# Performance work log

Measured on AMD Instinct MI355X. Metric: run time of the kernel, lower is better.

## Reference

```python
import jax, jax.numpy as jnp
import numpy as np
from jax import lax

SPAN = 11
K = 2 * SPAN + 1          # 23 -> 529 offsets
SIG_RGB = 0.1
SIG_XY = 6.0
LAM = 0.15
B, C, H, W = 2, 3, 160, 160


def _patches(x):
    """x: (N, C, H, W) -> (N, C, K, K, H, W), zero-padded.
    patch[di, dj] at pixel (i, j) equals x[i + di - SPAN, j + dj - SPAN],
    matching the torch module's shifted-slice double loop (dx = di - SPAN)."""
    n, c, h, w = x.shape
    xp = jnp.pad(x, ((0, 0), (0, 0), (SPAN, SPAN), (SPAN, SPAN)))

    def get(off):
        di = off // K
        dj = off % K
        return lax.dynamic_slice(xp, (0, 0, di, dj), (n, c, h, w))

    p = jax.vmap(get)(jnp.arange(K * K))              # (K*K, N, C, H, W)
    return p.reshape(K, K, n, c, h, w).transpose(2, 3, 0, 1, 4, 5)


def setup_inputs() -> dict:
    key = jax.random.key(0)
    k1, k2, k3, k4, k5 = jax.random.split(key, 5)
    logit = jax.random.normal(k1, (B, C, H, W), jnp.float32)
    target = jax.random.randint(k2, (B, H, W), 0, C)
    # small-magnitude image so exp(-0.5*(x - patch/0.1)^2) does not fully underflow
    image = jax.random.uniform(k3, (B, 3, H, W), jnp.float32) * 0.1
    source_map = (jax.random.uniform(k4, (B, 1, H, W)) > 0.5).astype(jnp.float32)
    destination_map = (jax.random.uniform(k5, (B, H, W)) > 0.5).astype(jnp.float32)
    return dict(logit=logit, target=target, image=image,
                source_map=source_map, destination_map=destination_map)


def _gcrf(image, y_hat, source_map, m_dst):
    b, c, h, w = y_hat.shape
    img_p = _patches(image)                                  # (B,3,K,K,H,W)
    valid = _patches(jnp.ones((1, 1, h, w), image.dtype))[0, 0]  # (K,K,H,W) in-bounds mask
    # NOTE: faithful to source bug: only the shifted feature is divided by sigma
    drgb = image[:, :, None, None] - img_p / SIG_RGB
    k_rgb = jnp.exp(-0.5 * jnp.sum(drgb * drgb, axis=1))     # (B,K,K,H,W)
    ii, jj = jnp.meshgrid(jnp.arange(h, dtype=image.dtype),
                          jnp.arange(w, dtype=image.dtype), indexing='ij')
    idx = jnp.stack([ii, jj])[None]                          # (1,2,H,W)
    idx_p = _patches(idx)[0]                                 # (2,K,K,H,W)
    dxy = idx[0][:, None, None] - idx_p / SIG_XY
    k_xy = jnp.exp(-0.5 * jnp.sum(dxy * dxy, axis=0))        # (K,K,H,W)
    kmat = (k_rgb + k_xy[None]) * valid[None]                # out-of-bounds offsets stay 0
    m_src = _patches(source_map)[:, 0]                       # (B,K,K,H,W)
    Kg = kmat * m_src * m_dst[:, None, None]                 # gated kernel
    U = _patches(y_hat)                                      # (B,C,K,K,H,W)
    Egy = jnp.einsum('bcijhw,bijhw->bchw', U, Kg)            # sum over window
    temp = jnp.einsum('bchw,bdhw->bcd', Egy, y_hat)          # (B,C,C)
    Moff = 1.0 - jnp.eye(c, dtype=y_hat.dtype)               # off-diagonal compatibility
    return jnp.sum(Moff * temp) / (b * h * w)


def reference(logit, target, image, source_map, destination_map):
    y_hat = jax.nn.softmax(logit, axis=1)
    m_dst = 1.0 - destination_map
    L_gcrf = _gcrf(image, y_hat, source_map, m_dst)
    logp = jax.nn.log_softmax(logit, axis=1)
    L_ce = -jnp.take_along_axis(logp, target[:, None], axis=1)[:, 0]  # (B,H,W)
    L_ce = jnp.mean(L_ce * destination_map)
    return L_ce + LAM * L_gcrf
```

## Files before the change

kernel.cpp:

```cpp
#include <hip/hip_runtime.h>

#define Bn 2
#define Cn 3
#define Hn 160
#define Wn 160
#define SPANc 11
#define Kc 23
#define HWn (Hn * Wn)
#define PW 182
#define PP (PW * PW)
#define LAMc 0.15f
#define INVN (1.0f / (float)(Bn * HWn))
#define TJ 32
#define Gc 4
#define TI 32
#define NROW (TI + Kc - 1)
#define NREC (NROW * TJ)
#define CEXP (-0.72134752f)
#define CX   (14.42695041f)
#define CA   (0.72134752f)
#define NPREP ((Bn * PP + 255) / 256)

__device__ __forceinline__ float wave_reduce64(float v) {
#pragma unroll
    for (int off = 32; off > 0; off >>= 1) v += __shfl_down(v, off, 64);
    return v;
}

__device__ __forceinline__ unsigned int bf16pk(float a, float b) {
    unsigned int ua = __float_as_uint(a), ub = __float_as_uint(b);
    ua += 0x7fffu + ((ua >> 16) & 1u);
    ub += 0x7fffu + ((ub >> 16) & 1u);
    return (ua & 0xffff0000u) | (ub >> 16);
}

__global__ __launch_bounds__(256) void prep_kernel(
    const float* __restrict__ logit, const int* __restrict__ target,
    const float* __restrict__ image, const float* __restrict__ srcmap,
    const float* __restrict__ dstmap, uint4* __restrict__ gU4,
    float4* __restrict__ cvec, float* __restrict__ pc, float* __restrict__ out)
{
    int idx = blockIdx.x * 256 + threadIdx.x;
    float ce = 0.0f;
    if (idx < Bn * PP) {
        int b   = idx / PP;
        int rem = idx - b * PP;
        int ip  = rem / PW;
        int jp  = rem - ip * PW;
        int i = ip - SPANc, j = jp - SPANc;
        if ((unsigned)i < (unsigned)Hn && (unsigned)j < (unsigned)Wn) {
            int r = i * Wn + j;
            int p = b * HWn + r;
            const float* lg = logit + (size_t)b * Cn * HWn + r;
            float l0 = lg[0], l1 = lg[HWn], l2 = lg[2 * HWn];
            float m = fmaxf(l0, fmaxf(l1, l2));
            float e0 = __expf(l0 - m), e1 = __expf(l1 - m), e2 = __expf(l2 - m);
            float s = e0 + e1 + e2;
            float inv = 1.0f / s;
            float y0 = e0 * inv, y1 = e1 * inv, y2 = e2 * inv;
            float lse = m + __logf(s);

            const float* im = image + (size_t)b * 3 * HWn + r;
            float p0 = im[0], p1 = im[HWn], p2 = im[2 * HWn];
            float sv = srcmap[p];
            float dv = dstmap[p];

            float B = (p0 * p0 + p1 * p1 + p2 * p2) * (100.0f * CA);
            gU4[idx] = make_uint4(bf16pk(p0, p1), bf16pk(p2, -B),
                                  bf16pk(sv * y0, sv * y1), bf16pk(sv * y2, 0.0f));

            float md = LAMc * (1.0f - dv) * INVN;
            cvec[p] = make_float4(md * (1.0f - y0), md * (1.0f - y1),
                                  md * (1.0f - y2), 0.0f);

            int t = target[p];
            float lt = (t == 0) ? l0 : ((t == 1) ? l1 : l2);
            ce = (lse - lt) * dv * INVN;
        } else {
            gU4[idx] = make_uint4(0u, 0u, 0u, 0u);
        }
    }
    if (idx == 0) out[0] = 0.0f;

    float v = wave_reduce64(ce);
    __shared__ float wsum[4];
    int tid = threadIdx.x;
    if ((tid & 63) == 0) wsum[tid >> 6] = v;
    __syncthreads();
    if (tid == 0) pc[blockIdx.x] = wsum[0] + wsum[1] + wsum[2] + wsum[3];
}

template<bool XY>
__device__ __forceinline__ void tap(float p0, float p1, float p2, float mB,
                                    float q0, float q1, float q2,
                                    float c0s, float c1s, float c2s, float mA,
                                    bool xy_on, float dy2, float dxv,
                                    float& e0, float& e1, float& e2)
{
    float e = fmaf(c0s, p0, fmaf(c1s, p1, fmaf(c2s, p2, mB)));
    float k = exp2f(e + mA);
    if constexpr (XY) {
        if (xy_on) k += exp2f(fmaf(dxv, dxv, dy2) * CEXP);
    }
    e0 = fmaf(k, q0, e0);
    e1 = fmaf(k, q1, e1);
    e2 = fmaf(k, q2, e2);
}

template<bool XY>
__device__ __forceinline__ void window_loop(
    const uint4* sU4, int lbase,
    const float* c0s, const float* c1s, const float* c2s, const float* mA,
    bool xy_on, float dy2, float fi0, float eg[Gc][3])
{
#pragma unroll
    for (int r = 0; r < 3; ++r) {
        uint4 ru = sU4[lbase + r * TJ];
        float p0 = __uint_as_float(ru.x & 0xffff0000u);
        float p1 = __uint_as_float(ru.x << 16);
        float p2 = __uint_as_float(ru.y & 0xffff0000u);
        float mB = __uint_as_float(ru.y << 16);
        float q0 = __uint_as_float(ru.z & 0xffff0000u);
        float q1 = __uint_as_float(ru.z << 16);
        float q2 = __uint_as_float(ru.w & 0xffff0000u);
        float dxb = XY ? (fi0 - (fi0 + (float)(r - SPANc)) * (1.0f / 6.0f)) : 0.0f;
#pragma unroll
        for (int c = 0; c < 3; ++c) {
            if (c > r) continue;
            tap<XY>(p0, p1, p2, mB, q0, q1, q2, c0s[c], c1s[c], c2s[c], mA[c],
                    xy_on, dy2, dxb + (float)c, eg[c][0], eg[c][1], eg[c][2]);
        }
    }
#pragma unroll 2
    for (int r = 3; r <= 22; ++r) {
        uint4 ru = sU4[lbase + r * TJ];
        float p0 = __uint_as_float(ru.x & 0xffff0000u);
        float p1 = __uint_as_float(ru.x << 16);
        float p2 = __uint_as_float(ru.y & 0xffff0000u);
        float mB = __uint_as_float(ru.y << 16);
        float q0 = __uint_as_float(ru.z & 0xffff0000u);
        float q1 = __uint_as_float(ru.z << 16);
        float q2 = __uint_as_float(ru.w & 0xffff0000u);
        float dxb = XY ? (fi0 - (fi0 + (float)(r - SPANc)) * (1.0f / 6.0f)) : 0.0f;
#pragma unroll
        for (int c = 0; c < Gc; ++c) {
            tap<XY>(p0, p1, p2, mB, q0, q1, q2, c0s[c], c1s[c], c2s[c], mA[c],
                    xy_on, dy2, dxb + (float)c, eg[c][0], eg[c][1], eg[c][2]);
        }
    }
#pragma unroll
    for (int r = 23; r <= 25; ++r) {
        uint4 ru = sU4[lbase + r * TJ];
        float p0 = __uint_as_float(ru.x & 0xffff0000u);
        float p1 = __uint_as_float(ru.x << 16);
        float p2 = __uint_as_float(ru.y & 0xffff0000u);
        float mB = __uint_as_float(ru.y << 16);
        float q0 = __uint_as_float(ru.z & 0xffff0000u);
        float q1 = __uint_as_float(ru.z << 16);
        float q2 = __uint_as_float(ru.w & 0xffff0000u);
        float dxb = XY ? (fi0 - (fi0 + (float)(r - SPANc)) * (1.0f / 6.0f)) : 0.0f;
#pragma unroll
        for (int c = 1; c < Gc; ++c) {
            if (c < r - 22) continue;
            tap<XY>(p0, p1, p2, mB, q0, q1, q2, c0s[c], c1s[c], c2s[c], mA[c],
                    xy_on, dy2, dxb + (float)c, eg[c][0], eg[c][1], eg[c][2]);
        }
    }
}

__global__ __launch_bounds__(256, 4) void gcrf_kernel(
    const uint4* __restrict__ gU4, const float4* __restrict__ cvec,
    const float* __restrict__ pc, float* __restrict__ out)
{
    __shared__ uint4 sU4[NREC];

    int tx = threadIdx.x;
    int ty = threadIdx.y;
    int tid = ty * TJ + tx;
    int jx = blockIdx.x;
    int j  = jx * TJ + tx;
    int by = blockIdx.y;
    int b  = by / 5;
    int it = by - b * 5;
    int i0g = it * TI + ty * Gc;
    int dj = blockIdx.z;

    size_t g0 = (size_t)b * PP + (size_t)(it * TI) * PW + (jx * TJ + dj);
    for (int n = tid; n < NREC; n += 256) {
        int rr = n >> 5, cc = n & 31;
        sU4[n] = gU4[g0 + (size_t)rr * PW + cc];
    }
    __syncthreads();

    int lbase = ty * Gc * TJ + tx;
    float c0s[Gc], c1s[Gc], c2s[Gc], mA[Gc];
#pragma unroll
    for (int c = 0; c < Gc; ++c) {
        uint4 cu = sU4[lbase + (c + SPANc) * TJ];
        float cc0 = __uint_as_float(cu.x & 0xffff0000u);
        float cc1 = __uint_as_float(cu.x << 16);
        float cc2 = __uint_as_float(cu.y & 0xffff0000u);
        c0s[c] = cc0 * CX; c1s[c] = cc1 * CX; c2s[c] = cc2 * CX;
        mA[c] = -CA * fmaf(cc0, cc0, fmaf(cc1, cc1, cc2 * cc2));
    }

    bool xy_on = (j < 16) && (i0g < 16);
    float dy = (float)j - (float)(j + dj - SPANc) * (1.0f / 6.0f);
    float dy2 = dy * dy;
    float fi0 = (float)i0g;

    float eg[Gc][3];
#pragma unroll
    for (int c = 0; c < Gc; ++c) { eg[c][0] = 0.f; eg[c][1] = 0.f; eg[c][2] = 0.f; }

    if (jx == 0 && it == 0) {
        window_loop<true>(sU4, lbase, c0s, c1s, c2s, mA, xy_on, dy2, fi0, eg);
    } else {
        window_loop<false>(sU4, lbase, c0s, c1s, c2s, mA, false, dy2, fi0, eg);
    }

    const float4* cv = cvec + ((size_t)b * HWn + (size_t)i0g * Wn + j);
    float contrib = 0.0f;
#pragma unroll
    for (int c = 0; c < Gc; ++c) {
        float4 t = cv[(size_t)c * Wn];
        contrib += eg[c][0] * t.x + eg[c][1] * t.y + eg[c][2] * t.z;
    }

    float v = wave_reduce64(contrib);
    __shared__ float wsum[4];
    if ((tid & 63) == 0) wsum[tid >> 6] = v;
    __syncthreads();
    if (tid == 0) atomicAdd(out, wsum[0] + wsum[1] + wsum[2] + wsum[3]);

    if (jx == 4 && by == 9 && dj == 22) {
        float s = 0.0f;
        if (tid < NPREP) s += pc[tid];
        if (tid + 256 < NPREP) s += pc[tid + 256];
        float v2 = wave_reduce64(s);
        __syncthreads();
        if ((tid & 63) == 0) wsum[tid >> 6] = v2;
        __syncthreads();
        if (tid == 0) atomicAdd(out, wsum[0] + wsum[1] + wsum[2] + wsum[3]);
    }
}

extern "C" void kernel_launch(void* const* d_in, const int* in_sizes, int n_in,
                              void* d_out, int out_size, void* d_ws, size_t ws_size,
                              hipStream_t stream)
{
    const float* logit  = (const float*)d_in[0];
    const int*   target = (const int*)d_in[1];
    const float* image  = (const float*)d_in[2];
    const float* srcmap = (const float*)d_in[3];
    const float* dstmap = (const float*)d_in[4];
    float* out = (float*)d_out;

    const size_t NRECG = (size_t)Bn * PP;
    float*  pc   = (float*)((char*)d_ws + 256);
    uint4*  gU4  = (uint4*)((char*)d_ws + 4096);
    float4* cvec = (float4*)((char*)d_ws + 4096 + NRECG * 16);

    prep_kernel<<<NPREP, 256, 0, stream>>>(logit, target, image, srcmap, dstmap,
                                           gU4, cvec, pc, out);
    dim3 grid(Wn / TJ, (Hn / TI) * Bn, Kc);
    dim3 blk(TJ, 8);
    gcrf_kernel<<<grid, blk, 0, stream>>>(gU4, cvec, pc, out);
}
```

Before: 85.23 us.

## Process two horizontal window offsets per block to amortize tile loads

Each block now handles two adjacent column offsets (dj0, dj0+1), loading a 33-column shared tile instead of a 32-column one. The grid's z dimension drops from 23 to 12, with the last slice handling a single offset. Center-pixel coefficients are read from global memory instead of shared memory. This halves the block count and the shared-memory fill and setup overhead per offset, at the cost of a longer per-thread loop with more register pressure and a 33-column shared stride.

```diff
diff --git a/kernel.cpp b/kernel.cpp
--- a/kernel.cpp
+++ b/kernel.cpp
@@ -15,7 +15,8 @@
 #define Gc 4
 #define TI 32
 #define NROW (TI + Kc - 1)
-#define NREC (NROW * TJ)
+#define NCOL2 (TJ + 1)
+#define NRECP (NROW * NCOL2)
 #define CEXP (-0.72134752f)
 #define CX   (14.42695041f)
 #define CA   (0.72134752f)
@@ -107,124 +108,149 @@
     e2 = fmaf(k, q2, e2);
 }
 
-template<bool XY>
-__device__ __forceinline__ void window_loop(
-    const uint4* sU4, int lbase,
-    const float* c0s, const float* c1s, const float* c2s, const float* mA,
-    bool xy_on, float dy2, float fi0, float eg[Gc][3])
-{
+template<bool XY, int DJN>
+__device__ __forceinline__ float body(
+    const uint4* __restrict__ gU4, const float4* __restrict__ cvec,
+    uint4* sU4, int b, int it, int jx, int dj0, int tx, int ty, int tid)
+{
+    const int NCOLt = TJ + DJN - 1;
+    const int NRECt = NROW * NCOLt;
+    size_t g0 = (size_t)b * PP + (size_t)(it * TI) * PW + (jx * TJ + dj0);
+    for (int n = tid; n < NRECt; n += 256) {
+        int rr = n / NCOLt, cc = n - rr * NCOLt;
+        sU4[n] = gU4[g0 + (size_t)rr * PW + cc];
+    }
+    __syncthreads();
+
+    int j = jx * TJ + tx;
+    int i0g = it * TI + ty * Gc;
+
+    float c0s[Gc], c1s[Gc], c2s[Gc], mA[Gc];
+    {
+        size_t crow = (size_t)b * PP + (size_t)(i0g + SPANc) * PW + (j + SPANc);
+#pragma unroll
+        for (int c = 0; c < Gc; ++c) {
+            uint4 cu = gU4[crow + (size_t)c * PW];
+            float cc0 = __uint_as_float(cu.x & 0xffff0000u);
+            float cc1 = __uint_as_float(cu.x << 16);
+            float cc2 = __uint_as_float(cu.y & 0xffff0000u);
+            c0s[c] = cc0 * CX; c1s[c] = cc1 * CX; c2s[c] = cc2 * CX;
+            mA[c] = -CA * fmaf(cc0, cc0, fmaf(cc1, cc1, cc2 * cc2));
+        }
+    }
+
+    bool xy_on = (j < 16) && (i0g < 16);
+    float fi0 = (float)i0g;
+    float dy2v[DJN];
+#pragma unroll
+    for (int d = 0; d < DJN; ++d) {
+        float dy = (float)j - (float)(j + dj0 + d - SPANc) * (1.0f / 6.0f);
+        dy2v[d] = dy * dy;
+    }
+
+    float eg[Gc][3];
+#pragma unroll
+    for (int c = 0; c < Gc; ++c) { eg[c][0] = 0.f; eg[c][1] = 0.f; eg[c][2] = 0.f; }
+
+    int lbase = ty * Gc * NCOLt + tx;
+
 #pragma unroll
     for (int r = 0; r < 3; ++r) {
-        uint4 ru = sU4[lbase + r * TJ];
-        float p0 = __uint_as_float(ru.x & 0xffff0000u);
-        float p1 = __uint_as_float(ru.x << 16);
-        float p2 = __uint_as_float(ru.y & 0xffff0000u);
-        float mB = __uint_as_float(ru.y << 16);
-        float q0 = __uint_as_float(ru.z & 0xffff0000u);
-        float q1 = __uint_as_float(ru.z << 16);
-        float q2 = __uint_as_float(ru.w & 0xffff0000u);
         float dxb = XY ? (fi0 - (fi0 + (float)(r - SPANc)) * (1.0f / 6.0f)) : 0.0f;
 #pragma unroll
-        for (int c = 0; c < 3; ++c) {
-            if (c > r) continue;
-            tap<XY>(p0, p1, p2, mB, q0, q1, q2, c0s[c], c1s[c], c2s[c], mA[c],
-                    xy_on, dy2, dxb + (float)c, eg[c][0], eg[c][1], eg[c][2]);
+        for (int d = 0; d < DJN; ++d) {
+            uint4 ru = sU4[lbase + r * NCOLt + d];
+            float p0 = __uint_as_float(ru.x & 0xffff0000u);
+            float p1 = __uint_as_float(ru.x << 16);
+            float p2 = __uint_as_float(ru.y & 0xffff0000u);
+            float mB = __uint_as_float(ru.y << 16);
+            float q0 = __uint_as_float(ru.z & 0xffff0000u);
+            float q1 = __uint_as_float(ru.z << 16);
+            float q2 = __uint_as_float(ru.w & 0xffff0000u);
+#pragma unroll
+            for (int c = 0; c < 3; ++c) {
+                if (c > r) continue;
+                tap<XY>(p0, p1, p2, mB, q0, q1, q2, c0s[c], c1s[c], c2s[c], mA[c],
+                        xy_on, dy2v[d], dxb + (float)c, eg[c][0], eg[c][1], eg[c][2]);
+            }
         }
     }
 #pragma unroll 2
     for (int r = 3; r <= 22; ++r) {
-        uint4 ru = sU4[lbase + r * TJ];
-        float p0 = __uint_as_float(ru.x & 0xffff0000u);
-        float p1 = __uint_as_float(ru.x << 16);
-        float p2 = __uint_as_float(ru.y & 0xffff0000u);
-        float mB = __uint_as_float(ru.y << 16);
-        float q0 = __uint_as_float(ru.z & 0xffff0000u);
-        float q1 = __uint_as_float(ru.z << 16);
-        float q2 = __uint_as_float(ru.w & 0xffff0000u);
         float dxb = XY ? (fi0 - (fi0 + (float)(r - SPANc)) * (1.0f / 6.0f)) : 0.0f;
 #pragma unroll
-        for (int c = 0; c < Gc; ++c) {
-            tap<XY>(p0, p1, p2, mB, q0, q1, q2, c0s[c], c1s[c], c2s[c], mA[c],
-                    xy_on, dy2, dxb + (float)c, eg[c][0], eg[c][1], eg[c][2]);
+        for (int d = 0; d < DJN; ++d) {
+            uint4 ru = sU4[lbase + r * NCOLt + d];
+            float p0 = __uint_as_float(ru.x & 0xffff0000u);
+            float p1 = __uint_as_float(ru.x << 16);
+            float p2 = __uint_as_float(ru.y & 0xffff0000u);
+            float mB = __uint_as_float(ru.y << 16);
+            float q0 = __uint_as_float(ru.z & 0xffff0000u);
+            float q1 = __uint_as_float(ru.z << 16);
+            float q2 = __uint_as_float(ru.w & 0xffff0000u);
+#pragma unroll
+            for (int c = 0; c < Gc; ++c) {
+                tap<XY>(p0, p1, p2, mB, q0, q1, q2, c0s[c], c1s[c], c2s[c], mA[c],
+                        xy_on, dy2v[d], dxb + (float)c, eg[c][0], eg[c][1], eg[c][2]);
+            }
         }
     }
 #pragma unroll
     for (int r = 23; r <= 25; ++r) {
-        uint4 ru = sU4[lbase + r * TJ];
-        float p0 = __uint_as_float(ru.x & 0xffff0000u);
-        float p1 = __uint_as_float(ru.x << 16);
-        float p2 = __uint_as_float(ru.y & 0xffff0000u);
-        float mB = __uint_as_float(ru.y << 16);
-        float q0 = __uint_as_float(ru.z & 0xffff0000u);
-        float q1 = __uint_as_float(ru.z << 16);
-        float q2 = __uint_as_float(ru.w & 0xffff0000u);
         float dxb = XY ? (fi0 - (fi0 + (float)(r - SPANc)) * (1.0f / 6.0f)) : 0.0f;
 #pragma unroll
-        for (int c = 1; c < Gc; ++c) {
-            if (c < r - 22) continue;
-            tap<XY>(p0, p1, p2, mB, q0, q1, q2, c0s[c], c1s[c], c2s[c], mA[c],
-                    xy_on, dy2, dxb + (float)c, eg[c][0], eg[c][1], eg[c][2]);
-        }
-    }
+        for (int d = 0; d < DJN; ++d) {
+            uint4 ru = sU4[lbase + r * NCOLt + d];
+            float p0 = __uint_as_float(ru.x & 0xffff0000u);
+            float p1 = __uint_as_float(ru.x << 16);
+            float p2 = __uint_as_float(ru.y & 0xffff0000u);
+            float mB = __uint_as_float(ru.y << 16);
+            float q0 = __uint_as_float(ru.z & 0xffff0000u);
+            float q1 = __uint_as_float(ru.z << 16);
+            float q2 = __uint_as_float(ru.w & 0xffff0000u);
+#pragma unroll
+            for (int c = 1; c < Gc; ++c) {
+                if (c < r - 22) continue;
+                tap<XY>(p0, p1, p2, mB, q0, q1, q2, c0s[c], c1s[c], c2s[c], mA[c],
+                        xy_on, dy2v[d], dxb + (float)c, eg[c][0], eg[c][1], eg[c][2]);
+            }
+        }
+    }
+
+    const float4* cv = cvec + ((size_t)b * HWn + (size_t)i0g * Wn + j);
+    float contrib = 0.0f;
+#pragma unroll
+    for (int c = 0; c < Gc; ++c) {
+        float4 t = cv[(size_t)c * Wn];
+        contrib += eg[c][0] * t.x + eg[c][1] * t.y + eg[c][2] * t.z;
+    }
+    return contrib;
 }
 
 __global__ __launch_bounds__(256, 4) void gcrf_kernel(
     const uint4* __restrict__ gU4, const float4* __restrict__ cvec,
     const float* __restrict__ pc, float* __restrict__ out)
 {
-    __shared__ uint4 sU4[NREC];
+    __shared__ uint4 sU4[NRECP];
 
     int tx = threadIdx.x;
     int ty = threadIdx.y;
     int tid = ty * TJ + tx;
     int jx = blockIdx.x;
-    int j  = jx * TJ + tx;
     int by = blockIdx.y;
     int b  = by / 5;
     int it = by - b * 5;
-    int i0g = it * TI + ty * Gc;
-    int dj = blockIdx.z;
-
-    size_t g0 = (size_t)b * PP + (size_t)(it * TI) * PW + (jx * TJ + dj);
-    for (int n = tid; n < NREC; n += 256) {
-        int rr = n >> 5, cc = n & 31;
-        sU4[n] = gU4[g0 + (size_t)rr * PW + cc];
-    }
-    __syncthreads();
-
-    int lbase = ty * Gc * TJ + tx;
-    float c0s[Gc], c1s[Gc], c2s[Gc], mA[Gc];
-#pragma unroll
-    for (int c = 0; c < Gc; ++c) {
-        uint4 cu = sU4[lbase + (c + SPANc) * TJ];
-        float cc0 = __uint_as_float(cu.x & 0xffff0000u);
-        float cc1 = __uint_as_float(cu.x << 16);
-        float cc2 = __uint_as_float(cu.y & 0xffff0000u);
-        c0s[c] = cc0 * CX; c1s[c] = cc1 * CX; c2s[c] = cc2 * CX;
-        mA[c] = -CA * fmaf(cc0, cc0, fmaf(cc1, cc1, cc2 * cc2));
-    }
-
-    bool xy_on = (j < 16) && (i0g < 16);
-    float dy = (float)j - (float)(j + dj - SPANc) * (1.0f / 6.0f);
-    float dy2 = dy * dy;
-    float fi0 = (float)i0g;
-
-    float eg[Gc][3];
-#pragma unroll
-    for (int c = 0; c < Gc; ++c) { eg[c][0] = 0.f; eg[c][1] = 0.f; eg[c][2] = 0.f; }
-
-    if (jx == 0 && it == 0) {
-        window_loop<true>(sU4, lbase, c0s, c1s, c2s, mA, xy_on, dy2, fi0, eg);
+    int z  = blockIdx.z;
+    int dj0 = 2 * z;
+
+    bool xyb = (jx == 0 && it == 0);
+    float contrib;
+    if (z == 11) {
+        contrib = xyb ? body<true, 1>(gU4, cvec, sU4, b, it, jx, dj0, tx, ty, tid)
+                      : body<false, 1>(gU4, cvec, sU4, b, it, jx, dj0, tx, ty, tid);
     } else {
-        window_loop<false>(sU4, lbase, c0s, c1s, c2s, mA, false, dy2, fi0, eg);
-    }
-
-    const float4* cv = cvec + ((size_t)b * HWn + (size_t)i0g * Wn + j);
-    float contrib = 0.0f;
-#pragma unroll
-    for (int c = 0; c < Gc; ++c) {
-        float4 t = cv[(size_t)c * Wn];
-        contrib += eg[c][0] * t.x + eg[c][1] * t.y + eg[c][2] * t.z;
+        contrib = xyb ? body<true, 2>(gU4, cvec, sU4, b, it, jx, dj0, tx, ty, tid)
+                      : body<false, 2>(gU4, cvec, sU4, b, it, jx, dj0, tx, ty, tid);
     }
 
     float v = wave_reduce64(contrib);
@@ -233,7 +259,7 @@
     __syncthreads();
     if (tid == 0) atomicAdd(out, wsum[0] + wsum[1] + wsum[2] + wsum[3]);
 
-    if (jx == 4 && by == 9 && dj == 22) {
+    if (jx == 4 && by == 9 && z == 11) {
         float s = 0.0f;
         if (tid < NPREP) s += pc[tid];
         if (tid + 256 < NPREP) s += pc[tid + 256];
@@ -263,7 +289,7 @@
 
     prep_kernel<<<NPREP, 256, 0, stream>>>(logit, target, image, srcmap, dstmap,
                                            gU4, cvec, pc, out);
-    dim3 grid(Wn / TJ, (Hn / TI) * Bn, Kc);
+    dim3 grid(Wn / TJ, (Hn / TI) * Bn, 12);
     dim3 blk(TJ, 8);
     gcrf_kernel<<<grid, blk, 0, stream>>>(gU4, cvec, pc, out);
 }
```

Result: no change. 85.96 us (+0.9%).
